# Kernel optimization log

Measured on AMD Instinct MI355X. Metric: run time of the kernel, lower is better.

The kernel has to match this reference:

```python
import jax, jax.numpy as jnp
import numpy as np

IN_DIM, H_DIM, OUT_DIM, N_LAYERS = 512, 1024, 512, 2


def _linear_params(key, out_d, in_d, bias=True):
    k1, k2 = jax.random.split(key)
    bound = 1.0 / np.sqrt(in_d)
    W = jax.random.uniform(k1, (out_d, in_d), jnp.float32, -bound, bound)
    if bias:
        b = jax.random.uniform(k2, (out_d,), jnp.float32, -bound, bound)
        return W, b
    return (W,)


def setup_inputs() -> dict:
    key = jax.random.key(0)
    keys = jax.random.split(key, 32)
    inp = {"x": jax.random.normal(keys[0], (32, 512, IN_DIM), jnp.float32)}
    ki = 1
    for layer in range(N_LAYERS):
        lin = IN_DIM if layer == 0 else H_DIM
        for gate in ("z", "r", "g"):
            W, b = _linear_params(keys[ki], H_DIM, lin); ki += 1
            inp[f"Wx{gate}{layer}"] = W
            inp[f"bx{gate}{layer}"] = b
            (Wh,) = _linear_params(keys[ki], H_DIM, H_DIM, bias=False); ki += 1
            inp[f"Wh{gate}{layer}"] = Wh
    Why, bhy = _linear_params(keys[ki], OUT_DIM, H_DIM)
    inp["Why"] = Why
    inp["bhy"] = bhy
    return inp


def _gru_forward(x, layers, Why, bhy):
    B = x.shape[0]
    h0 = tuple(jnp.zeros((B, H_DIM), x.dtype) for _ in range(N_LAYERS))

    def cell(p, h_prev, xin):
        Wxz, bxz, Whz, Wxr, bxr, Whr, Wxg, bxg, Whg = p
        z = jax.nn.sigmoid(xin @ Wxz.T + bxz + h_prev @ Whz.T)
        r = jax.nn.sigmoid(xin @ Wxr.T + bxr + h_prev @ Whr.T)
        g = jnp.tanh(xin @ Wxg.T + bxg + (r * h_prev) @ Whg.T)
        return z * h_prev + (1.0 - z) * g

    def step(hs, xt):
        cur = xt
        new_hs = []
        for p, h in zip(layers, hs):
            h_new = cell(p, h, cur)
            new_hs.append(h_new)
            cur = h_new
        yt = cur @ Why.T + bhy  # (B, O)
        return tuple(new_hs), yt

    xs = jnp.swapaxes(x, 0, 1)  # (S, B, I)
    final_hs, ys = jax.lax.scan(step, h0, xs)
    layer_output = jnp.swapaxes(ys, 0, 1)  # (B, S, O)
    hidden_state = jnp.stack(final_hs, axis=1)  # (B, L, H)
    return layer_output, hidden_state


def reference(x,
              Wxz0, bxz0, Whz0, Wxr0, bxr0, Whr0, Wxg0, bxg0, Whg0,
              Wxz1, bxz1, Whz1, Wxr1, bxr1, Whr1, Wxg1, bxg1, Whg1,
              Why, bhy):
    layers = [
        (Wxz0, bxz0, Whz0, Wxr0, bxr0, Whr0, Wxg0, bxg0, Whg0),
        (Wxz1, bxz1, Whz1, Wxr1, bxr1, Whr1, Wxg1, bxg1, Whg1),
    ]
    return _gru_forward(x, layers, Why, bhy)
```

## Files before the change

kernel.cpp:

```cpp
#include <hip/hip_runtime.h>

#define SS 512
#define NWG 52
#define NTHR 512
#define NITER 517
#define OUT_HID_OFF 8388608

typedef _Float16 fh8 __attribute__((ext_vector_type(8)));
typedef float f32x4 __attribute__((ext_vector_type(4)));

struct GP {
  const float *x;
  const float *Wxz0,*bxz0,*Whz0,*Wxr0,*bxr0,*Whr0,*Wxg0,*bxg0,*Whg0;
  const float *Wxz1,*bxz1,*Whz1,*Wxr1,*bxr1,*Whr1,*Wxg1,*bxg1,*Whg1;
  const float *Why,*bhy;
  float *out;
  _Float16 *xb;
  _Float16 *wzr0,*wzr1,*wg0,*wg1,*wy;
  float *h0f,*h1f;
  _Float16 *h0h,*h1h;
  float *z0,*z1;
  _Float16 *r0,*r1;
  unsigned *fg0,*fg1;
  unsigned *flags;
};

__device__ __forceinline__ float aloadf(const float* p) {
  return __hip_atomic_load(p, __ATOMIC_RELAXED, __HIP_MEMORY_SCOPE_AGENT);
}
__device__ __forceinline__ void astore(float* p, float v) {
  __hip_atomic_store(p, v, __ATOMIC_RELAXED, __HIP_MEMORY_SCOPE_AGENT);
}
__device__ __forceinline__ void bload(uint4& d, const void* p) {
  asm volatile("global_load_dwordx4 %0, %1, off sc0 sc1"
               : "=&v"(d) : "v"(p) : "memory");
}
__device__ __forceinline__ void bload1(float& d, const float* p) {
  asm volatile("global_load_dword %0, %1, off sc0 sc1"
               : "=&v"(d) : "v"(p) : "memory");
}
__device__ __forceinline__ void sstore(_Float16* pd, float v) {
  _Float16 h = (_Float16)v;
  unsigned short u; __builtin_memcpy(&u, &h, 2);
  asm volatile("global_store_short %0, %1, off sc0 sc1"
               :: "v"(pd), "v"((unsigned)u) : "memory");
}
__device__ __forceinline__ fh8 u2h(uint4 v){ fh8 r; __builtin_memcpy(&r, &v, 16); return r; }
__device__ __forceinline__ uint4 h2u(fh8 v){ uint4 r; __builtin_memcpy(&r, &v, 16); return r; }
__device__ __forceinline__ float sigmf(float v){ return 1.f/(1.f+__expf(-v)); }

__global__ __launch_bounds__(256) void pack(GP p) {
  const long gid = (long)blockIdx.x*256 + threadIdx.x;
  if (gid < 1441792) {
    long u; int KC; _Float16* dst;
    if (gid < 393216)       { u=gid;         KC=48; dst=p.wzr0; }
    else if (gid < 917504)  { u=gid-393216;  KC=64; dst=p.wzr1; }
    else if (gid < 1114112) { u=gid-917504;  KC=48; dst=p.wg0;  }
    else if (gid < 1376256) { u=gid-1114112; KC=64; dst=p.wg1;  }
    else                    { u=gid-1376256; KC=32; dst=p.wy;   }
    const int per = KC*64;
    const int ntg = (int)(u/per); const int r = (int)(u%per);
    const int kc = r>>6, lane = r&63;
    const int n = ntg*16 + (lane&15);
    const int k = kc*32 + ((lane>>4)<<3);
    const float* src;
    if (gid < 393216) {
      int g = n>>10, nn = n&1023;
      src = (k<512) ? ((g?p.Wxr0:p.Wxz0) + (size_t)nn*512 + k)
                    : ((g?p.Whr0:p.Whz0) + (size_t)nn*1024 + (k-512));
    } else if (gid < 917504) {
      int g = n>>10, nn = n&1023;
      src = (k<1024) ? ((g?p.Wxr1:p.Wxz1) + (size_t)nn*1024 + k)
                     : ((g?p.Whr1:p.Whz1) + (size_t)nn*1024 + (k-1024));
    } else if (gid < 1114112) {
      src = (k<512) ? (p.Wxg0 + (size_t)n*512 + k)
                    : (p.Whg0 + (size_t)n*1024 + (k-512));
    } else if (gid < 1376256) {
      src = (k<1024) ? (p.Wxg1 + (size_t)n*1024 + k)
                     : (p.Whg1 + (size_t)n*1024 + (k-1024));
    } else {
      src = p.Why + (size_t)n*1024 + k;
    }
    float4 f0 = *(const float4*)src, f1 = *(const float4*)(src+4);
    fh8 h;
    h[0]=(_Float16)f0.x; h[1]=(_Float16)f0.y; h[2]=(_Float16)f0.z; h[3]=(_Float16)f0.w;
    h[4]=(_Float16)f1.x; h[5]=(_Float16)f1.y; h[6]=(_Float16)f1.z; h[7]=(_Float16)f1.w;
    *(fh8*)(dst + u*8) = h;
  } else if (gid < 2490368) {
    const long e = (gid - 1441792)*8;
    float4 f0 = *(const float4*)(p.x + e), f1 = *(const float4*)(p.x + e + 4);
    fh8 h;
    h[0]=(_Float16)f0.x; h[1]=(_Float16)f0.y; h[2]=(_Float16)f0.z; h[3]=(_Float16)f0.w;
    h[4]=(_Float16)f1.x; h[5]=(_Float16)f1.y; h[6]=(_Float16)f1.z; h[7]=(_Float16)f1.w;
    *(fh8*)(p.xb + e) = h;
  }
}

__device__ __forceinline__ void gridbar(unsigned* flags, unsigned g) {
  asm volatile("s_waitcnt vmcnt(0) lgkmcnt(0)" ::: "memory");
  __syncthreads();
  if (threadIdx.x == 0)
    __hip_atomic_store(flags + (size_t)blockIdx.x*32, g,
                       __ATOMIC_RELAXED, __HIP_MEMORY_SCOPE_AGENT);
  if (threadIdx.x < NWG) {
    const unsigned* f = flags + (size_t)threadIdx.x*32;
    while (__hip_atomic_load(f, __ATOMIC_RELAXED, __HIP_MEMORY_SCOPE_AGENT) < g)
      __builtin_amdgcn_s_sleep(1);
  }
  asm volatile("" ::: "memory");
  __syncthreads();
}

__device__ __forceinline__ void wait8(const unsigned* fb, unsigned g) {
  if (threadIdx.x < 8) {
    const unsigned* f = fb + (size_t)threadIdx.x*32;
    while (__hip_atomic_load(f, __ATOMIC_RELAXED, __HIP_MEMORY_SCOPE_AGENT) < g)
      __builtin_amdgcn_s_sleep(1);
  }
  asm volatile("" ::: "memory");
  __syncthreads();
}

__device__ __forceinline__ void issue_copy(uint4* R, const _Float16* base, int row, int s16) {
  const char* sp = (const char*)(base + (size_t)row*1024) + s16*64;
  bload(R[0], sp); bload(R[1], sp+16); bload(R[2], sp+32); bload(R[3], sp+48);
}
__device__ __forceinline__ void issue_prod(uint4* Ra, uint4* Rh,
    const _Float16* ra, const _Float16* ha, int row, int s16) {
  const char* rp = (const char*)(ra + (size_t)row*1024) + s16*64;
  const char* hp = (const char*)(ha + (size_t)row*1024) + s16*64;
  #pragma unroll
  for (int q = 0; q < 4; ++q) { bload(Ra[q], rp + q*16); bload(Rh[q], hp + q*16); }
}
__device__ __forceinline__ void issue_x(uint4* R, const _Float16* xab, int row, int s16) {
  const uint4* sp = (const uint4*)(xab + (size_t)row*262144 + (size_t)s16*32);
  R[0]=sp[0]; R[1]=sp[1]; R[2]=sp[2]; R[3]=sp[3];
}
__device__ __forceinline__ void commit4(const uint4* R, char* As, int s, int row, int s16) {
  const int key = (row & 15) << 4;
  char* d = As + (size_t)row*4096;
  const int kb0 = s*1024 + s16*64;
  #pragma unroll
  for (int q = 0; q < 4; ++q) *(uint4*)(d + ((kb0 + q*16) ^ key)) = R[q];
}
__device__ __forceinline__ void commit_prod(const uint4* Ra, const uint4* Rh,
    char* As, int s, int row, int s16) {
  const int key = (row & 15) << 4;
  char* d = As + (size_t)row*4096;
  const int kb0 = s*1024 + s16*64;
  #pragma unroll
  for (int q = 0; q < 4; ++q) {
    fh8 o = u2h(Ra[q]) * u2h(Rh[q]);
    *(uint4*)(d + ((kb0 + q*16) ^ key)) = h2u(o);
  }
}

__device__ __forceinline__ void sweep_range(const char* As, const _Float16* wpk,
    int ntg, int KC, int k0, int k1, int l, f32x4& acc0, f32x4& acc1) {
  const int lrow = l & 15, key = lrow << 4, lg16 = (l >> 4) << 4;
  const char* ab = As + (size_t)lrow*4096;
  const _Float16* wb = wpk + (size_t)ntg*KC*512 + (size_t)l*8;
  #pragma unroll 8
  for (int kk = k0; kk < k1; ++kk) {
    const int off = (kk*64 + lg16) ^ key;
    fh8 a0 = *(const fh8*)(ab + off);
    fh8 a1 = *(const fh8*)(ab + 16*4096 + off);
    fh8 b  = *(const fh8*)(wb + (size_t)kk*512);
    acc0 = __builtin_amdgcn_mfma_f32_16x16x32_f16(a0, b, acc0, 0, 0, 0);
    acc1 = __builtin_amdgcn_mfma_f32_16x16x32_f16(a1, b, acc1, 0, 0, 0);
  }
}

__device__ __forceinline__ void epi_zr(const f32x4& a0, const f32x4& a1, int ntg, int l,
    const float* bz, const float* br, float* zbuf, _Float16* rbuf) {
  const int col = (ntg << 4) | (l & 15);
  const int gate = col >> 10, cc = col & 1023;
  const float bias = gate ? br[cc] : bz[cc];
  const int brow = (l >> 4) << 2;
  #pragma unroll
  for (int q = 0; q < 4; ++q) {
    const float v0 = sigmf(a0[q]+bias), v1 = sigmf(a1[q]+bias);
    if (gate) {
      sstore(rbuf + (size_t)(brow+q)*1024 + cc, v0);
      sstore(rbuf + (size_t)(brow+q+16)*1024 + cc, v1);
    } else {
      astore(zbuf + (size_t)(brow+q)*1024 + cc, v0);
      astore(zbuf + (size_t)(brow+q+16)*1024 + cc, v1);
    }
  }
}
__device__ __forceinline__ void epi_h(const f32x4& a0, const f32x4& a1, int colB, int brow,
    const float* bgp, const float* zv, const float* hv, float* hF, _Float16* hH) {
  const float bias = bgp[colB];
  #pragma unroll
  for (int q = 0; q < 4; ++q) {
    { const float g = tanhf(a0[q]+bias);
      const float hn = zv[q]*hv[q] + (1.f-zv[q])*g;
      astore(hF + (size_t)(brow+q)*1024 + colB, hn);
      sstore(hH + (size_t)(brow+q)*1024 + colB, hn); }
    { const float g = tanhf(a1[q]+bias);
      const float hn = zv[4+q]*hv[4+q] + (1.f-zv[4+q])*g;
      astore(hF + (size_t)(brow+q+16)*1024 + colB, hn);
      sstore(hH + (size_t)(brow+q+16)*1024 + colB, hn); }
  }
}

__global__ __launch_bounds__(NTHR, 2) void gru_main(GP p) {
  __shared__ char As[131072];
  const int tid = threadIdx.x, wg = blockIdx.x;
  const int wid = tid >> 6, l = tid & 63;
  const int row = tid >> 4, s16 = tid & 15;
  const int brow = (l >> 4) << 2;
  unsigned gen = 0;

  for (int i = 0; i < NITER; ++i) {
    if (wg < 16) {
      if (i <= 511) {
        const int t = i;
        const int ntg = wg*8 + wid;
        f32x4 a0 = {0.f,0.f,0.f,0.f}, a1 = {0.f,0.f,0.f,0.f};
        { uint4 Rx[4];
          issue_x(Rx, p.xb + (size_t)t*512, row, s16);
          commit4(Rx, As, 0, row, s16); }
        __syncthreads();
        sweep_range(As, p.wzr0, ntg, 48, 0, 16, l, a0, a1);
        if (t >= 1) wait8(p.fg0, (unsigned)i);
        { const _Float16* hb = p.h0h + (size_t)((t-1)&3)*32768;
          uint4 R0[4], R1[4];
          issue_copy(R0, hb, row, s16);
          issue_copy(R1, hb+512, row, s16);
          asm volatile("s_waitcnt vmcnt(0)" ::: "memory");
          __builtin_amdgcn_sched_barrier(0);
          commit4(R0, As, 1, row, s16);
          commit4(R1, As, 2, row, s16); }
        __syncthreads();
        sweep_range(As, p.wzr0, ntg, 48, 16, 48, l, a0, a1);
        epi_zr(a0, a1, ntg, l, p.bxz0, p.bxr0,
               p.z0 + (size_t)(t&1)*32768, p.r0 + (size_t)(t&1)*32768);
      }
    } else if (wg < 32) {
      if (i >= 2 && i <= 513) {
        const int t1 = i-2;
        const int ntg = (wg-16)*8 + wid;
        f32x4 a0 = {0.f,0.f,0.f,0.f}, a1 = {0.f,0.f,0.f,0.f};
        { const _Float16* hb = p.h0h + (size_t)(t1&3)*32768;
          uint4 R0[4], R1[4];
          issue_copy(R0, hb, row, s16);
          issue_copy(R1, hb+512, row, s16);
          asm volatile("s_waitcnt vmcnt(0)" ::: "memory");
          __builtin_amdgcn_sched_barrier(0);
          commit4(R0, As, 0, row, s16);
          commit4(R1, As, 1, row, s16); }
        __syncthreads();
        sweep_range(As, p.wzr1, ntg, 64, 0, 32, l, a0, a1);
        if (t1 >= 1) wait8(p.fg1, (unsigned)i);
        { const _Float16* hb = p.h1h + (size_t)((t1-1)&3)*32768;
          uint4 R0[4], R1[4];
          issue_copy(R0, hb, row, s16);
          issue_copy(R1, hb+512, row, s16);
          asm volatile("s_waitcnt vmcnt(0)" ::: "memory");
          __builtin_amdgcn_sched_barrier(0);
          commit4(R0, As, 2, row, s16);
          commit4(R1, As, 3, row, s16); }
        __syncthreads();
        sweep_range(As, p.wzr1, ntg, 64, 32, 64, l, a0, a1);
        epi_zr(a0, a1, ntg, l, p.bxz1, p.bxr1,
               p.z1 + (size_t)(t1&1)*32768, p.r1 + (size_t)(t1&1)*32768);
      }
    } else if (wg < 40) {
      if (i >= 1 && i <= 512) {
        const int u = i-1;
        const int ntg = (wg-32)*8 + wid;
        const int colB = (ntg << 4) | (l & 15);
        const float*    zr    = p.z0  + (size_t)(u&1)*32768;
        const float*    hfold = p.h0f + (size_t)((u-1)&3)*32768;
        const _Float16* rr    = p.r0  + (size_t)(u&1)*32768;
        const _Float16* hh    = p.h0h + (size_t)((u-1)&3)*32768;
        float zv[8], hv[8];
        uint4 Rx[4], Ra[8], Rh[8];
        issue_x(Rx, p.xb + (size_t)u*512, row, s16);
        issue_prod(&Ra[0], &Rh[0], rr, hh, row, s16);
        issue_prod(&Ra[4], &Rh[4], rr+512, hh+512, row, s16);
        #pragma unroll
        for (int q = 0; q < 4; ++q) {
          bload1(zv[q],   zr    + (size_t)(brow+q)*1024 + colB);
          bload1(zv[4+q], zr    + (size_t)(brow+q+16)*1024 + colB);
          bload1(hv[q],   hfold + (size_t)(brow+q)*1024 + colB);
          bload1(hv[4+q], hfold + (size_t)(brow+q+16)*1024 + colB);
        }
        asm volatile("s_waitcnt vmcnt(0)" ::: "memory");
        __builtin_amdgcn_sched_barrier(0);
        commit4(Rx, As, 0, row, s16);
        commit_prod(&Ra[0], &Rh[0], As, 1, row, s16);
        commit_prod(&Ra[4], &Rh[4], As, 2, row, s16);
        __syncthreads();
        f32x4 a0 = {0.f,0.f,0.f,0.f}, a1 = {0.f,0.f,0.f,0.f};
        sweep_range(As, p.wg0, ntg, 48, 0, 48, l, a0, a1);
        epi_h(a0, a1, colB, brow, p.bxg0, zv, hv,
              p.h0f + (size_t)(u&3)*32768, p.h0h + (size_t)(u&3)*32768);
        asm volatile("s_waitcnt vmcnt(0) lgkmcnt(0)" ::: "memory");
        __syncthreads();
        if (tid == 0)
          __hip_atomic_store(p.fg0 + (size_t)(wg-32)*32, (unsigned)i,
                             __ATOMIC_RELAXED, __HIP_MEMORY_SCOPE_AGENT);
      }
    } else if (wg < 48) {
      if (i >= 3 && i <= 514) {
        const int v = i-3;
        const int ntg = (wg-40)*8 + wid;
        const int colB = (ntg << 4) | (l & 15);
        const float*    zr    = p.z1  + (size_t)(v&1)*32768;
        const float*    hfold = p.h1f + (size_t)((v-1)&3)*32768;
        const _Float16* rr    = p.r1  + (size_t)(v&1)*32768;
        const _Float16* hh1   = p.h1h + (size_t)((v-1)&3)*32768;
        const _Float16* h0in  = p.h0h + (size_t)(v&3)*32768;
        float zv[8], hv[8];
        uint4 Rf[8], Ra[8], Rh[8];
        issue_copy(&Rf[0], h0in, row, s16);
        issue_copy(&Rf[4], h0in+512, row, s16);
        issue_prod(&Ra[0], &Rh[0], rr, hh1, row, s16);
        issue_prod(&Ra[4], &Rh[4], rr+512, hh1+512, row, s16);
        #pragma unroll
        for (int q = 0; q < 4; ++q) {
          bload1(zv[q],   zr    + (size_t)(brow+q)*1024 + colB);
          bload1(zv[4+q], zr    + (size_t)(brow+q+16)*1024 + colB);
          bload1(hv[q],   hfold + (size_t)(brow+q)*1024 + colB);
          bload1(hv[4+q], hfold + (size_t)(brow+q+16)*1024 + colB);
        }
        asm volatile("s_waitcnt vmcnt(0)" ::: "memory");
        __builtin_amdgcn_sched_barrier(0);
        commit4(&Rf[0], As, 0, row, s16);
        commit4(&Rf[4], As, 1, row, s16);
        commit_prod(&Ra[0], &Rh[0], As, 2, row, s16);
        commit_prod(&Ra[4], &Rh[4], As, 3, row, s16);
        __syncthreads();
        f32x4 a0 = {0.f,0.f,0.f,0.f}, a1 = {0.f,0.f,0.f,0.f};
        sweep_range(As, p.wg1, ntg, 64, 0, 64, l, a0, a1);
        epi_h(a0, a1, colB, brow, p.bxg1, zv, hv,
              p.h1f + (size_t)(v&3)*32768, p.h1h + (size_t)(v&3)*32768);
        asm volatile("s_waitcnt vmcnt(0) lgkmcnt(0)" ::: "memory");
        __syncthreads();
        if (tid == 0)
          __hip_atomic_store(p.fg1 + (size_t)(wg-40)*32, (unsigned)i,
                             __ATOMIC_RELAXED, __HIP_MEMORY_SCOPE_AGENT);
      }
    } else {
      if (i >= 5) {
        const int w = i-5;
        const int ntg = (wg-48)*8 + wid;
        const _Float16* hb = p.h1h + (size_t)(w&3)*32768;
        uint4 R0[4], R1[4];
        issue_copy(R0, hb, row, s16);
        issue_copy(R1, hb+512, row, s16);
        asm volatile("s_waitcnt vmcnt(0)" ::: "memory");
        __builtin_amdgcn_sched_barrier(0);
        commit4(R0, As, 0, row, s16);
        commit4(R1, As, 1, row, s16);
        __syncthreads();
        f32x4 a0 = {0.f,0.f,0.f,0.f}, a1 = {0.f,0.f,0.f,0.f};
        sweep_range(As, p.wy, ntg, 32, 0, 32, l, a0, a1);
        const int col = (ntg << 4) | (l & 15);
        const float bias = p.bhy[col];
        #pragma unroll
        for (int q = 0; q < 4; ++q) {
          p.out[(size_t)(brow+q)*262144    + (size_t)w*512 + col] = a0[q] + bias;
          p.out[(size_t)(brow+q+16)*262144 + (size_t)w*512 + col] = a1[q] + bias;
        }
      }
    }
    gridbar(p.flags, ++gen);
  }

  for (int e = wg*NTHR + tid; e < 65536; e += NWG*NTHR) {
    const int b = e >> 11, r2 = e & 2047, lay = r2 >> 10, hcol = r2 & 1023;
    const float* hb = (lay ? p.h1f : p.h0f) + (size_t)3*32768 + b*1024 + hcol;
    p.out[OUT_HID_OFF + (size_t)b*2048 + (size_t)lay*1024 + hcol] = aloadf(hb);
  }
}

extern "C" void kernel_launch(void* const* d_in, const int* in_sizes, int n_in,
                              void* d_out, int out_size, void* d_ws, size_t ws_size,
                              hipStream_t stream) {
  GP P;
  P.x    = (const float*)d_in[0];
  P.Wxz0 = (const float*)d_in[1];  P.bxz0 = (const float*)d_in[2];  P.Whz0 = (const float*)d_in[3];
  P.Wxr0 = (const float*)d_in[4];  P.bxr0 = (const float*)d_in[5];  P.Whr0 = (const float*)d_in[6];
  P.Wxg0 = (const float*)d_in[7];  P.bxg0 = (const float*)d_in[8];  P.Whg0 = (const float*)d_in[9];
  P.Wxz1 = (const float*)d_in[10]; P.bxz1 = (const float*)d_in[11]; P.Whz1 = (const float*)d_in[12];
  P.Wxr1 = (const float*)d_in[13]; P.bxr1 = (const float*)d_in[14]; P.Whr1 = (const float*)d_in[15];
  P.Wxg1 = (const float*)d_in[16]; P.bxg1 = (const float*)d_in[17]; P.Whg1 = (const float*)d_in[18];
  P.Why  = (const float*)d_in[19]; P.bhy  = (const float*)d_in[20];
  P.out  = (float*)d_out;

  char* ws = (char*)d_ws;
  P.xb   = (_Float16*)(ws + 0);
  P.wzr0 = (_Float16*)(ws + 16777216);
  P.wzr1 = (_Float16*)(ws + 23068672);
  P.wg0  = (_Float16*)(ws + 31457280);
  P.wg1  = (_Float16*)(ws + 34603008);
  P.wy   = (_Float16*)(ws + 38797312);
  P.h0f  = (float*)   (ws + 39845888);
  P.h1f  = (float*)   (ws + 40370176);
  P.h0h  = (_Float16*)(ws + 40894464);
  P.h1h  = (_Float16*)(ws + 41156608);
  P.z0   = (float*)   (ws + 41418752);
  P.z1   = (float*)   (ws + 41680896);
  P.r0   = (_Float16*)(ws + 41943040);
  P.r1   = (_Float16*)(ws + 42074112);
  P.fg0  = (unsigned*)(ws + 42205184);
  P.fg1  = (unsigned*)(ws + 42206208);
  P.flags= (unsigned*)(ws + 42207232);

  hipMemsetAsync(ws + 39845888, 0, 42213888 - 39845888, stream);

  pack<<<dim3(9728), dim3(256), 0, stream>>>(P);

  void* args[] = { &P };
  hipError_t err = hipLaunchCooperativeKernel((const void*)gru_main,
                                              dim3(NWG), dim3(NTHR), args, 0, stream);
  if (err != hipSuccess) {
    (void)hipGetLastError();
    gru_main<<<dim3(NWG), dim3(NTHR), 0, stream>>>(P);
  }
}
```

Before: 9.771 ms.

## Replace global grid barrier with per-stage producer/consumer flags in GRU pipeline

Drops the per-iteration grid-wide barrier across all 52 workgroups. Each role group now runs its own time loop and waits only on the specific flags it depends on (z/r, h, and output-stage progress), with ring-buffer depth guards. The g-workgroups also start the x-part of the gate GEMM before waiting, keep the previous hidden state in registers instead of reloading it, and write the final hidden state directly. This removes lockstep stalls between stages, but correctness now depends on the flag-distance checks being right for the 4-slot and 2-slot buffers.

```diff
diff --git a/kernel.cpp b/kernel.cpp
--- a/kernel.cpp
+++ b/kernel.cpp
@@ -3,7 +3,6 @@
 #define SS 512
 #define NWG 52
 #define NTHR 512
-#define NITER 517
 #define OUT_HID_OFF 8388608
 
 typedef _Float16 fh8 __attribute__((ext_vector_type(8)));
@@ -22,12 +21,10 @@
   float *z0,*z1;
   _Float16 *r0,*r1;
   unsigned *fg0,*fg1;
-  unsigned *flags;
+  unsigned *fzr0,*fzr1;
+  unsigned *fy;
 };
 
-__device__ __forceinline__ float aloadf(const float* p) {
-  return __hip_atomic_load(p, __ATOMIC_RELAXED, __HIP_MEMORY_SCOPE_AGENT);
-}
 __device__ __forceinline__ void astore(float* p, float v) {
   __hip_atomic_store(p, v, __ATOMIC_RELAXED, __HIP_MEMORY_SCOPE_AGENT);
 }
@@ -96,29 +93,22 @@
   }
 }
 
-__device__ __forceinline__ void gridbar(unsigned* flags, unsigned g) {
+__device__ __forceinline__ void waitf(const unsigned* fb, int n, int need) {
+  if (need > 0) {
+    if ((int)threadIdx.x < n) {
+      const unsigned* f = fb + (size_t)threadIdx.x*32;
+      while ((int)__hip_atomic_load(f, __ATOMIC_RELAXED, __HIP_MEMORY_SCOPE_AGENT) < need)
+        __builtin_amdgcn_s_sleep(1);
+    }
+    asm volatile("" ::: "memory");
+    __syncthreads();
+  }
+}
+__device__ __forceinline__ void setflag(unsigned* f, unsigned v) {
   asm volatile("s_waitcnt vmcnt(0) lgkmcnt(0)" ::: "memory");
   __syncthreads();
   if (threadIdx.x == 0)
-    __hip_atomic_store(flags + (size_t)blockIdx.x*32, g,
-                       __ATOMIC_RELAXED, __HIP_MEMORY_SCOPE_AGENT);
-  if (threadIdx.x < NWG) {
-    const unsigned* f = flags + (size_t)threadIdx.x*32;
-    while (__hip_atomic_load(f, __ATOMIC_RELAXED, __HIP_MEMORY_SCOPE_AGENT) < g)
-      __builtin_amdgcn_s_sleep(1);
-  }
-  asm volatile("" ::: "memory");
-  __syncthreads();
-}
-
-__device__ __forceinline__ void wait8(const unsigned* fb, unsigned g) {
-  if (threadIdx.x < 8) {
-    const unsigned* f = fb + (size_t)threadIdx.x*32;
-    while (__hip_atomic_load(f, __ATOMIC_RELAXED, __HIP_MEMORY_SCOPE_AGENT) < g)
-      __builtin_amdgcn_s_sleep(1);
-  }
-  asm volatile("" ::: "memory");
-  __syncthreads();
+    __hip_atomic_store(f, v, __ATOMIC_RELAXED, __HIP_MEMORY_SCOPE_AGENT);
 }
 
 __device__ __forceinline__ void issue_copy(uint4* R, const _Float16* base, int row, int s16) {
@@ -189,21 +179,6 @@
     }
   }
 }
-__device__ __forceinline__ void epi_h(const f32x4& a0, const f32x4& a1, int colB, int brow,
-    const float* bgp, const float* zv, const float* hv, float* hF, _Float16* hH) {
-  const float bias = bgp[colB];
-  #pragma unroll
-  for (int q = 0; q < 4; ++q) {
-    { const float g = tanhf(a0[q]+bias);
-      const float hn = zv[q]*hv[q] + (1.f-zv[q])*g;
-      astore(hF + (size_t)(brow+q)*1024 + colB, hn);
-      sstore(hH + (size_t)(brow+q)*1024 + colB, hn); }
-    { const float g = tanhf(a1[q]+bias);
-      const float hn = zv[4+q]*hv[4+q] + (1.f-zv[4+q])*g;
-      astore(hF + (size_t)(brow+q+16)*1024 + colB, hn);
-      sstore(hH + (size_t)(brow+q+16)*1024 + colB, hn); }
-  }
-}
 
 __global__ __launch_bounds__(NTHR, 2) void gru_main(GP p) {
   __shared__ char As[131072];
@@ -211,170 +186,210 @@
   const int wid = tid >> 6, l = tid & 63;
   const int row = tid >> 4, s16 = tid & 15;
   const int brow = (l >> 4) << 2;
-  unsigned gen = 0;
-
-  for (int i = 0; i < NITER; ++i) {
-    if (wg < 16) {
-      if (i <= 511) {
-        const int t = i;
-        const int ntg = wg*8 + wid;
-        f32x4 a0 = {0.f,0.f,0.f,0.f}, a1 = {0.f,0.f,0.f,0.f};
-        { uint4 Rx[4];
-          issue_x(Rx, p.xb + (size_t)t*512, row, s16);
-          commit4(Rx, As, 0, row, s16); }
-        __syncthreads();
-        sweep_range(As, p.wzr0, ntg, 48, 0, 16, l, a0, a1);
-        if (t >= 1) wait8(p.fg0, (unsigned)i);
-        { const _Float16* hb = p.h0h + (size_t)((t-1)&3)*32768;
-          uint4 R0[4], R1[4];
-          issue_copy(R0, hb, row, s16);
-          issue_copy(R1, hb+512, row, s16);
-          asm volatile("s_waitcnt vmcnt(0)" ::: "memory");
-          __builtin_amdgcn_sched_barrier(0);
-          commit4(R0, As, 1, row, s16);
-          commit4(R1, As, 2, row, s16); }
-        __syncthreads();
-        sweep_range(As, p.wzr0, ntg, 48, 16, 48, l, a0, a1);
-        epi_zr(a0, a1, ntg, l, p.bxz0, p.bxr0,
-               p.z0 + (size_t)(t&1)*32768, p.r0 + (size_t)(t&1)*32768);
-      }
-    } else if (wg < 32) {
-      if (i >= 2 && i <= 513) {
-        const int t1 = i-2;
-        const int ntg = (wg-16)*8 + wid;
-        f32x4 a0 = {0.f,0.f,0.f,0.f}, a1 = {0.f,0.f,0.f,0.f};
-        { const _Float16* hb = p.h0h + (size_t)(t1&3)*32768;
-          uint4 R0[4], R1[4];
-          issue_copy(R0, hb, row, s16);
-          issue_copy(R1, hb+512, row, s16);
-          asm volatile("s_waitcnt vmcnt(0)" ::: "memory");
-          __builtin_amdgcn_sched_barrier(0);
-          commit4(R0, As, 0, row, s16);
-          commit4(R1, As, 1, row, s16); }
-        __syncthreads();
-        sweep_range(As, p.wzr1, ntg, 64, 0, 32, l, a0, a1);
-        if (t1 >= 1) wait8(p.fg1, (unsigned)i);
-        { const _Float16* hb = p.h1h + (size_t)((t1-1)&3)*32768;
-          uint4 R0[4], R1[4];
-          issue_copy(R0, hb, row, s16);
-          issue_copy(R1, hb+512, row, s16);
-          asm volatile("s_waitcnt vmcnt(0)" ::: "memory");
-          __builtin_amdgcn_sched_barrier(0);
-          commit4(R0, As, 2, row, s16);
-          commit4(R1, As, 3, row, s16); }
-        __syncthreads();
-        sweep_range(As, p.wzr1, ntg, 64, 32, 64, l, a0, a1);
-        epi_zr(a0, a1, ntg, l, p.bxz1, p.bxr1,
-               p.z1 + (size_t)(t1&1)*32768, p.r1 + (size_t)(t1&1)*32768);
-      }
-    } else if (wg < 40) {
-      if (i >= 1 && i <= 512) {
-        const int u = i-1;
-        const int ntg = (wg-32)*8 + wid;
-        const int colB = (ntg << 4) | (l & 15);
-        const float*    zr    = p.z0  + (size_t)(u&1)*32768;
-        const float*    hfold = p.h0f + (size_t)((u-1)&3)*32768;
-        const _Float16* rr    = p.r0  + (size_t)(u&1)*32768;
-        const _Float16* hh    = p.h0h + (size_t)((u-1)&3)*32768;
-        float zv[8], hv[8];
-        uint4 Rx[4], Ra[8], Rh[8];
+
+  if (wg < 16) {
+    const int ntg = wg*8 + wid;
+    for (int t = 0; t < SS; ++t) {
+      { uint4 Rx[4];
+        issue_x(Rx, p.xb + (size_t)t*512, row, s16);
+        commit4(Rx, As, 0, row, s16); }
+      __syncthreads();
+      f32x4 a0 = {0.f,0.f,0.f,0.f}, a1 = {0.f,0.f,0.f,0.f};
+      sweep_range(As, p.wzr0, ntg, 48, 0, 16, l, a0, a1);
+      waitf(p.fg0, 8, t);
+      { const _Float16* hb = p.h0h + (size_t)((t-1)&3)*32768;
+        uint4 R0[4], R1[4];
+        issue_copy(R0, hb, row, s16);
+        issue_copy(R1, hb+512, row, s16);
+        asm volatile("s_waitcnt vmcnt(0)" ::: "memory");
+        __builtin_amdgcn_sched_barrier(0);
+        commit4(R0, As, 1, row, s16);
+        commit4(R1, As, 2, row, s16); }
+      __syncthreads();
+      sweep_range(As, p.wzr0, ntg, 48, 16, 48, l, a0, a1);
+      epi_zr(a0, a1, ntg, l, p.bxz0, p.bxr0,
+             p.z0 + (size_t)(t&1)*32768, p.r0 + (size_t)(t&1)*32768);
+      setflag(p.fzr0 + (size_t)wg*32, (unsigned)(t+1));
+    }
+  } else if (wg < 32) {
+    const int ntg = (wg-16)*8 + wid;
+    for (int t = 0; t < SS; ++t) {
+      waitf(p.fg0, 8, t+1);
+      { const _Float16* hb = p.h0h + (size_t)(t&3)*32768;
+        uint4 R0[4], R1[4];
+        issue_copy(R0, hb, row, s16);
+        issue_copy(R1, hb+512, row, s16);
+        asm volatile("s_waitcnt vmcnt(0)" ::: "memory");
+        __builtin_amdgcn_sched_barrier(0);
+        commit4(R0, As, 0, row, s16);
+        commit4(R1, As, 1, row, s16); }
+      __syncthreads();
+      f32x4 a0 = {0.f,0.f,0.f,0.f}, a1 = {0.f,0.f,0.f,0.f};
+      sweep_range(As, p.wzr1, ntg, 64, 0, 32, l, a0, a1);
+      waitf(p.fg1, 8, t);
+      { const _Float16* hb = p.h1h + (size_t)((t-1)&3)*32768;
+        uint4 R0[4], R1[4];
+        issue_copy(R0, hb, row, s16);
+        issue_copy(R1, hb+512, row, s16);
+        asm volatile("s_waitcnt vmcnt(0)" ::: "memory");
+        __builtin_amdgcn_sched_barrier(0);
+        commit4(R0, As, 2, row, s16);
+        commit4(R1, As, 3, row, s16); }
+      __syncthreads();
+      sweep_range(As, p.wzr1, ntg, 64, 32, 64, l, a0, a1);
+      epi_zr(a0, a1, ntg, l, p.bxz1, p.bxr1,
+             p.z1 + (size_t)(t&1)*32768, p.r1 + (size_t)(t&1)*32768);
+      setflag(p.fzr1 + (size_t)(wg-16)*32, (unsigned)(t+1));
+    }
+  } else if (wg < 40) {
+    const int gi = wg - 32;
+    const int ntg = gi*8 + wid;
+    const int colB = (ntg << 4) | (l & 15);
+    const float biasB = p.bxg0[colB];
+    float hv[8];
+    #pragma unroll
+    for (int q = 0; q < 8; ++q) hv[q] = 0.f;
+    for (int u = 0; u < SS; ++u) {
+      { uint4 Rx[4];
         issue_x(Rx, p.xb + (size_t)u*512, row, s16);
+        commit4(Rx, As, 0, row, s16); }
+      __syncthreads();
+      f32x4 a0 = {0.f,0.f,0.f,0.f}, a1 = {0.f,0.f,0.f,0.f};
+      sweep_range(As, p.wg0, ntg, 48, 0, 16, l, a0, a1);
+      waitf(p.fzr0, 16, u+1);
+      waitf(p.fg0,  8,  u);
+      waitf(p.fzr1, 16, u-3);
+      waitf(p.fg1,  8,  u-3);
+      { const float*    zr = p.z0 + (size_t)(u&1)*32768;
+        const _Float16* rr = p.r0 + (size_t)(u&1)*32768;
+        const _Float16* hh = p.h0h + (size_t)((u-1)&3)*32768;
+        float zv[8];
+        uint4 Ra[8], Rh[8];
         issue_prod(&Ra[0], &Rh[0], rr, hh, row, s16);
         issue_prod(&Ra[4], &Rh[4], rr+512, hh+512, row, s16);
         #pragma unroll
         for (int q = 0; q < 4; ++q) {
-          bload1(zv[q],   zr    + (size_t)(brow+q)*1024 + colB);
-          bload1(zv[4+q], zr    + (size_t)(brow+q+16)*1024 + colB);
-          bload1(hv[q],   hfold + (size_t)(brow+q)*1024 + colB);
-          bload1(hv[4+q], hfold + (size_t)(brow+q+16)*1024 + colB);
+          bload1(zv[q],   zr + (size_t)(brow+q)*1024 + colB);
+          bload1(zv[4+q], zr + (size_t)(brow+q+16)*1024 + colB);
         }
         asm volatile("s_waitcnt vmcnt(0)" ::: "memory");
         __builtin_amdgcn_sched_barrier(0);
-        commit4(Rx, As, 0, row, s16);
         commit_prod(&Ra[0], &Rh[0], As, 1, row, s16);
         commit_prod(&Ra[4], &Rh[4], As, 2, row, s16);
         __syncthreads();
-        f32x4 a0 = {0.f,0.f,0.f,0.f}, a1 = {0.f,0.f,0.f,0.f};
-        sweep_range(As, p.wg0, ntg, 48, 0, 48, l, a0, a1);
-        epi_h(a0, a1, colB, brow, p.bxg0, zv, hv,
-              p.h0f + (size_t)(u&3)*32768, p.h0h + (size_t)(u&3)*32768);
-        asm volatile("s_waitcnt vmcnt(0) lgkmcnt(0)" ::: "memory");
-        __syncthreads();
-        if (tid == 0)
-          __hip_atomic_store(p.fg0 + (size_t)(wg-32)*32, (unsigned)i,
-                             __ATOMIC_RELAXED, __HIP_MEMORY_SCOPE_AGENT);
-      }
-    } else if (wg < 48) {
-      if (i >= 3 && i <= 514) {
-        const int v = i-3;
-        const int ntg = (wg-40)*8 + wid;
-        const int colB = (ntg << 4) | (l & 15);
-        const float*    zr    = p.z1  + (size_t)(v&1)*32768;
-        const float*    hfold = p.h1f + (size_t)((v-1)&3)*32768;
-        const _Float16* rr    = p.r1  + (size_t)(v&1)*32768;
-        const _Float16* hh1   = p.h1h + (size_t)((v-1)&3)*32768;
-        const _Float16* h0in  = p.h0h + (size_t)(v&3)*32768;
-        float zv[8], hv[8];
-        uint4 Rf[8], Ra[8], Rh[8];
-        issue_copy(&Rf[0], h0in, row, s16);
-        issue_copy(&Rf[4], h0in+512, row, s16);
-        issue_prod(&Ra[0], &Rh[0], rr, hh1, row, s16);
-        issue_prod(&Ra[4], &Rh[4], rr+512, hh1+512, row, s16);
+        sweep_range(As, p.wg0, ntg, 48, 16, 48, l, a0, a1);
+        float* hF = p.h0f + (size_t)(u&3)*32768;
+        _Float16* hH = p.h0h + (size_t)(u&3)*32768;
         #pragma unroll
         for (int q = 0; q < 4; ++q) {
-          bload1(zv[q],   zr    + (size_t)(brow+q)*1024 + colB);
-          bload1(zv[4+q], zr    + (size_t)(brow+q+16)*1024 + colB);
-          bload1(hv[q],   hfold + (size_t)(brow+q)*1024 + colB);
-          bload1(hv[4+q], hfold + (size_t)(brow+q+16)*1024 + colB);
+          { const float g = tanhf(a0[q]+biasB);
+            const float hn = zv[q]*hv[q] + (1.f-zv[q])*g;
+            hv[q] = hn;
+            astore(hF + (size_t)(brow+q)*1024 + colB, hn);
+            sstore(hH + (size_t)(brow+q)*1024 + colB, hn); }
+          { const float g = tanhf(a1[q]+biasB);
+            const float hn = zv[4+q]*hv[4+q] + (1.f-zv[4+q])*g;
+            hv[4+q] = hn;
+            astore(hF + (size_t)(brow+q+16)*1024 + colB, hn);
+            sstore(hH + (size_t)(brow+q+16)*1024 + colB, hn); }
         }
-        asm volatile("s_waitcnt vmcnt(0)" ::: "memory");
-        __builtin_amdgcn_sched_barrier(0);
-        commit4(&Rf[0], As, 0, row, s16);
-        commit4(&Rf[4], As, 1, row, s16);
+      }
+      setflag(p.fg0 + (size_t)gi*32, (unsigned)(u+1));
+    }
+    #pragma unroll
+    for (int q = 0; q < 4; ++q) {
+      p.out[OUT_HID_OFF + (size_t)(brow+q)*2048 + colB]    = hv[q];
+      p.out[OUT_HID_OFF + (size_t)(brow+q+16)*2048 + colB] = hv[4+q];
+    }
+  } else if (wg < 48) {
+    const int gi = wg - 40;
+    const int ntg = gi*8 + wid;
+    const int colB = (ntg << 4) | (l & 15);
+    const float biasB = p.bxg1[colB];
+    float hv[8];
+    #pragma unroll
+    for (int q = 0; q < 8; ++q) hv[q] = 0.f;
+    for (int v = 0; v < SS; ++v) {
+      waitf(p.fg0, 8, v+1);
+      { const _Float16* hb = p.h0h + (size_t)(v&3)*32768;
+        uint4 R0[4], R1[4];
+        issue_copy(R0, hb, row, s16);
+        issue_copy(R1, hb+512, row, s16);
+        asm volatile("s_waitcnt vmcnt(0)" ::: "memory");
+        __builtin_amdgcn_sched_barrier(0);
+        commit4(R0, As, 0, row, s16);
+        commit4(R1, As, 1, row, s16); }
+      __syncthreads();
+      f32x4 a0 = {0.f,0.f,0.f,0.f}, a1 = {0.f,0.f,0.f,0.f};
+      sweep_range(As, p.wg1, ntg, 64, 0, 32, l, a0, a1);
+      waitf(p.fzr1, 16, v+1);
+      waitf(p.fg1,  8,  v);
+      waitf(p.fy,   4,  v-3);
+      { const float*    zr = p.z1 + (size_t)(v&1)*32768;
+        const _Float16* rr = p.r1 + (size_t)(v&1)*32768;
+        const _Float16* hh = p.h1h + (size_t)((v-1)&3)*32768;
+        float zv[8];
+        uint4 Ra[8], Rh[8];
+        issue_prod(&Ra[0], &Rh[0], rr, hh, row, s16);
+        issue_prod(&Ra[4], &Rh[4], rr+512, hh+512, row, s16);
+        #pragma unroll
+        for (int q = 0; q < 4; ++q) {
+          bload1(zv[q],   zr + (size_t)(brow+q)*1024 + colB);
+          bload1(zv[4+q], zr + (size_t)(brow+q+16)*1024 + colB);
+        }
+        asm volatile("s_waitcnt vmcnt(0)" ::: "memory");
+        __builtin_amdgcn_sched_barrier(0);
         commit_prod(&Ra[0], &Rh[0], As, 2, row, s16);
         commit_prod(&Ra[4], &Rh[4], As, 3, row, s16);
         __syncthreads();
-        f32x4 a0 = {0.f,0.f,0.f,0.f}, a1 = {0.f,0.f,0.f,0.f};
-        sweep_range(As, p.wg1, ntg, 64, 0, 64, l, a0, a1);
-        epi_h(a0, a1, colB, brow, p.bxg1, zv, hv,
-              p.h1f + (size_t)(v&3)*32768, p.h1h + (size_t)(v&3)*32768);
-        asm volatile("s_waitcnt vmcnt(0) lgkmcnt(0)" ::: "memory");
-        __syncthreads();
-        if (tid == 0)
-          __hip_atomic_store(p.fg1 + (size_t)(wg-40)*32, (unsigned)i,
-                             __ATOMIC_RELAXED, __HIP_MEMORY_SCOPE_AGENT);
+        sweep_range(As, p.wg1, ntg, 64, 32, 64, l, a0, a1);
+        float* hF = p.h1f + (size_t)(v&3)*32768;
+        _Float16* hH = p.h1h + (size_t)(v&3)*32768;
+        #pragma unroll
+        for (int q = 0; q < 4; ++q) {
+          { const float g = tanhf(a0[q]+biasB);
+            const float hn = zv[q]*hv[q] + (1.f-zv[q])*g;
+            hv[q] = hn;
+            astore(hF + (size_t)(brow+q)*1024 + colB, hn);
+            sstore(hH + (size_t)(brow+q)*1024 + colB, hn); }
+          { const float g = tanhf(a1[q]+biasB);
+            const float hn = zv[4+q]*hv[4+q] + (1.f-zv[4+q])*g;
+            hv[4+q] = hn;
+            astore(hF + (size_t)(brow+q+16)*1024 + colB, hn);
+            sstore(hH + (size_t)(brow+q+16)*1024 + colB, hn); }
+        }
       }
-    } else {
-      if (i >= 5) {
-        const int w = i-5;
-        const int ntg = (wg-48)*8 + wid;
-        const _Float16* hb = p.h1h + (size_t)(w&3)*32768;
+      setflag(p.fg1 + (size_t)gi*32, (unsigned)(v+1));
+    }
+    #pragma unroll
+    for (int q = 0; q < 4; ++q) {
+      p.out[OUT_HID_OFF + (size_t)(brow+q)*2048 + 1024 + colB]    = hv[q];
+      p.out[OUT_HID_OFF + (size_t)(brow+q+16)*2048 + 1024 + colB] = hv[4+q];
+    }
+  } else {
+    const int ntg = (wg-48)*8 + wid;
+    const int col = (ntg << 4) | (l & 15);
+    const float bias = p.bhy[col];
+    for (int w = 0; w < SS; ++w) {
+      waitf(p.fg1, 8, w+1);
+      { const _Float16* hb = p.h1h + (size_t)(w&3)*32768;
         uint4 R0[4], R1[4];
         issue_copy(R0, hb, row, s16);
         issue_copy(R1, hb+512, row, s16);
         asm volatile("s_waitcnt vmcnt(0)" ::: "memory");
         __builtin_amdgcn_sched_barrier(0);
         commit4(R0, As, 0, row, s16);
-        commit4(R1, As, 1, row, s16);
-        __syncthreads();
-        f32x4 a0 = {0.f,0.f,0.f,0.f}, a1 = {0.f,0.f,0.f,0.f};
-        sweep_range(As, p.wy, ntg, 32, 0, 32, l, a0, a1);
-        const int col = (ntg << 4) | (l & 15);
-        const float bias = p.bhy[col];
-        #pragma unroll
-        for (int q = 0; q < 4; ++q) {
-          p.out[(size_t)(brow+q)*262144    + (size_t)w*512 + col] = a0[q] + bias;
-          p.out[(size_t)(brow+q+16)*262144 + (size_t)w*512 + col] = a1[q] + bias;
-        }
+        commit4(R1, As, 1, row, s16); }
+      __syncthreads();
+      f32x4 a0 = {0.f,0.f,0.f,0.f}, a1 = {0.f,0.f,0.f,0.f};
+      sweep_range(As, p.wy, ntg, 32, 0, 32, l, a0, a1);
+      #pragma unroll
+      for (int q = 0; q < 4; ++q) {
+        p.out[(size_t)(brow+q)*262144    + (size_t)w*512 + col] = a0[q] + bias;
+        p.out[(size_t)(brow+q+16)*262144 + (size_t)w*512 + col] = a1[q] + bias;
       }
-    }
-    gridbar(p.flags, ++gen);
-  }
-
-  for (int e = wg*NTHR + tid; e < 65536; e += NWG*NTHR) {
-    const int b = e >> 11, r2 = e & 2047, lay = r2 >> 10, hcol = r2 & 1023;
-    const float* hb = (lay ? p.h1f : p.h0f) + (size_t)3*32768 + b*1024 + hcol;
-    p.out[OUT_HID_OFF + (size_t)b*2048 + (size_t)lay*1024 + hcol] = aloadf(hb);
+      setflag(p.fy + (size_t)(wg-48)*32, (unsigned)(w+1));
+    }
   }
 }
 
@@ -409,7 +424,9 @@
   P.r1   = (_Float16*)(ws + 42074112);
   P.fg0  = (unsigned*)(ws + 42205184);
   P.fg1  = (unsigned*)(ws + 42206208);
-  P.flags= (unsigned*)(ws + 42207232);
+  P.fzr0 = (unsigned*)(ws + 42207232);
+  P.fzr1 = (unsigned*)(ws + 42209280);
+  P.fy   = (unsigned*)(ws + 42211328);
 
   hipMemsetAsync(ws + 39845888, 0, 42213888 - 39845888, stream);
 
```

After: 7.825 ms. 19.9% less time.
